# Kernel tuning notes

Measured on AMD Instinct MI355X. Metric: run time of the kernel, lower is better.

## Reference

```python
import jax, jax.numpy as jnp
import numpy as np

R = 4          # args.search_range
D = 2 * R + 1  # window size per axis -> D*D = 81 output channels


def setup_inputs() -> dict:
    key = jax.random.key(0)
    k1, k2 = jax.random.split(key)
    B, C, H, W = 4, 128, 64, 128
    src = jax.random.normal(k1, (B, C, H, W), dtype=jnp.float32)
    tgt = jax.random.normal(k2, (B, C, H, W), dtype=jnp.float32)
    return {"src": src, "tgt": tgt}


def reference(src, tgt):
    # Faithful to the torch code: tgt is zero-padded by R on each spatial side,
    # then for output pixel (i, j) the window indices into the PADDED tensor are
    # I in [i-R, i+R], J in [j-R, j+R]. For i < R the index is negative, which in
    # torch wraps around -> reproduce with modular indexing.
    B, C, H, W = src.shape
    tp = jnp.pad(tgt, ((0, 0), (0, 0), (R, R), (R, R)))  # [B,C,H+2R,W+2R]
    Hp, Wp = H + 2 * R, W + 2 * R
    # col_idx[dj, j] = (j - R + dj) mod Wp
    col_idx = (jnp.arange(W)[None, :] - R + jnp.arange(D)[:, None]) % Wp  # [D,W]
    outs = []
    for di in range(D):  # small fixed loop over 9 row offsets
        row_idx = (jnp.arange(H) - R + di) % Hp        # [H]
        t_rows = tp[:, :, row_idx, :]                  # [B,C,H,Wp]
        t_win = t_rows[:, :, :, col_idx]               # [B,C,H,D,W]
        # channel-dot-product per pixel and per column offset
        outs.append(jnp.einsum('bchdw,bchw->bdhw', t_win, src))
    # channel ordering k = di*D + dj matches the original double loop over (I, J)
    return jnp.concatenate(outs, axis=1)  # [B, D*D, H, W]
```

## Files before the change

kernel.cpp:

```cpp
#include <hip/hip_runtime.h>
#include <stdint.h>

#define NB 4
#define NC 128
#define NH 64
#define NW 128
#define HW (NH * NW)
#define ND 9
#define NOUT (ND * ND)
#define PROW 1040

typedef __attribute__((ext_vector_type(8))) short short8;
typedef __attribute__((ext_vector_type(4))) float f32x4;

__device__ __forceinline__ ushort f2bf(float f) {
  uint u = __float_as_uint(f);
  u += 0x7FFFu + ((u >> 16) & 1u);
  return (ushort)(u >> 16);
}

__global__ __launch_bounds__(512, 2) void costvol_kernel(const float* __restrict__ src,
                                                         const float* __restrict__ tgt,
                                                         float* __restrict__ out) {
  __shared__ ushort srcP[16 * PROW];
  __shared__ ushort tgtP[2][16 * PROW];
  __shared__ float  outlds[ND * NW];

  const int tid  = threadIdx.x;
  const int lane = tid & 63;
  const int wave = tid >> 6;
  const int col  = lane & 15;
  const int g    = lane >> 4;

  const int xcd = blockIdx.x & 7;
  const int b   = xcd >> 1;
  const int h   = ((xcd & 1) << 5) | (blockIdx.x >> 3);

  const int sc = (tid >> 5) << 3;
  const int sn = (tid & 31) << 2;

  const float* sbase = src + (size_t)(b * NC) * HW;
  const float* tbase = tgt + (size_t)(b * NC) * HW;

  {
    float4 v[8];
#pragma unroll
    for (int j = 0; j < 8; ++j)
      v[j] = *(const float4*)(sbase + (size_t)(sc + j) * HW + h * NW + sn);
#pragma unroll
    for (int i = 0; i < 4; ++i) {
      short8 e;
#pragma unroll
      for (int j = 0; j < 8; ++j) e[j] = (short)f2bf(((const float*)&v[j])[i]);
      *(short8*)&srcP[(tid >> 5) * PROW + (sn + i) * 8] = e;
    }
  }
  {
    const int y0 = (h - 8 < 0) ? 0 : (h - 8);
    float4 v[8];
#pragma unroll
    for (int j = 0; j < 8; ++j)
      v[j] = *(const float4*)(tbase + (size_t)(sc + j) * HW + y0 * NW + sn);
#pragma unroll
    for (int i = 0; i < 4; ++i) {
      short8 e;
#pragma unroll
      for (int j = 0; j < 8; ++j) e[j] = (short)f2bf(((const float*)&v[j])[i]);
      *(short8*)&tgtP[0][(tid >> 5) * PROW + (sn + i) * 8] = e;
    }
  }
  __syncthreads();

  const int m0 = wave << 4;
  short8 A[4];
#pragma unroll
  for (int kk = 0; kk < 4; ++kk)
    A[kk] = *(const short8*)&srcP[(4 * kk + g) * PROW + (m0 + col) * 8];

  for (int di = 0; di < ND; ++di) {
    const int p = di & 1;
    const int y = h + di - 8;

    float4 v[8];
    const bool havenext = (di < 8);
    if (havenext) {
      const int yn = (y + 1 < 0) ? 0 : (y + 1);
#pragma unroll
      for (int j = 0; j < 8; ++j)
        v[j] = *(const float4*)(tbase + (size_t)(sc + j) * HW + yn * NW + sn);
    }

    if (y >= 0) {
      const ushort* tp = tgtP[p];
      short8 BD[4], BS[4];
#pragma unroll
      for (int kk = 0; kk < 4; ++kk)
        BD[kk] = *(const short8*)&tp[(4 * kk + g) * PROW + (m0 + col) * 8];
      if (wave) {
#pragma unroll
        for (int kk = 0; kk < 4; ++kk)
          BS[kk] = *(const short8*)&tp[(4 * kk + g) * PROW + (m0 - 16 + col) * 8];
      }

      f32x4 accD = {0.f, 0.f, 0.f, 0.f};
      f32x4 accS = {0.f, 0.f, 0.f, 0.f};
#pragma unroll
      for (int kk = 0; kk < 4; ++kk)
        accD = __builtin_amdgcn_mfma_f32_16x16x32_bf16(A[kk], BD[kk], accD, 0, 0, 0);
      if (wave) {
#pragma unroll
        for (int kk = 0; kk < 4; ++kk)
          accS = __builtin_amdgcn_mfma_f32_16x16x32_bf16(A[kk], BS[kk], accS, 0, 0, 0);
      }

#pragma unroll
      for (int q = 0; q < 4; ++q) {
        const int row = 4 * g + q;
        const int w   = m0 + row;
        const int djd = col - row + 8;
        if (djd >= 0 && djd <= 8)
          outlds[djd * NW + ((w + 4 * djd) & 127)] = accD[q];
        if (wave) {
          const int djs = col - row - 8;
          if (djs >= 0 && djs <= 8)
            outlds[djs * NW + ((w + 4 * djs) & 127)] = accS[q];
        }
      }
    }

    if (havenext) {
#pragma unroll
      for (int i = 0; i < 4; ++i) {
        short8 e;
#pragma unroll
        for (int j = 0; j < 8; ++j) e[j] = (short)f2bf(((const float*)&v[j])[i]);
        *(short8*)&tgtP[p ^ 1][(tid >> 5) * PROW + (sn + i) * 8] = e;
      }
    }

    __syncthreads();

    if (tid < ND * 32) {
      const int dj = tid >> 5;
      const int w  = (tid & 31) << 2;
      f32x4 o = *(const f32x4*)&outlds[dj * NW + ((w + 4 * dj) & 127)];
      const bool vb = (y >= 0);
#pragma unroll
      for (int i = 0; i < 4; ++i)
        if (!vb || (w + i + dj < 8)) o[i] = 0.f;
      *(f32x4*)(out + ((size_t)((b * NOUT + di * ND + dj) * NH + h)) * NW + w) = o;
    }
    __syncthreads();
  }
}

extern "C" void kernel_launch(void* const* d_in, const int* in_sizes, int n_in,
                              void* d_out, int out_size, void* d_ws, size_t ws_size,
                              hipStream_t stream) {
  const float* src = (const float*)d_in[0];
  const float* tgt = (const float*)d_in[1];
  float* out = (float*)d_out;
  costvol_kernel<<<dim3(NB * NH), dim3(512), 0, stream>>>(src, tgt, out);
}
```

Before: 87.32 us.

## Split into bf16 pre-conversion pass and per-row-offset cost volume kernel

Adds a first kernel that converts src and tgt to bf16 once into a workspace, laid out channel-interleaved per row plane. The cost volume kernel then launches one block per (batch, row, di) instead of one per (batch, row), loading its bf16 planes straight from global memory with no per-iteration staging or barriers. This removes the 9x redundant fp32 tgt loads and conversions and the serial di loop with its double buffering, and gives nine times more blocks for parallelism. In exchange it adds a second launch and a round trip of the converted data through the workspace.

```diff
diff --git a/kernel.cpp b/kernel.cpp
--- a/kernel.cpp
+++ b/kernel.cpp
@@ -8,7 +8,8 @@
 #define HW (NH * NW)
 #define ND 9
 #define NOUT (ND * ND)
-#define PROW 1040
+#define PLANE 16384
+#define TGT_OFF ((size_t)NB * NH * PLANE)
 
 typedef __attribute__((ext_vector_type(8))) short short8;
 typedef __attribute__((ext_vector_type(4))) float f32x4;
@@ -19,13 +20,39 @@
   return (ushort)(u >> 16);
 }
 
-__global__ __launch_bounds__(512, 2) void costvol_kernel(const float* __restrict__ src,
+__global__ __launch_bounds__(512, 2) void convert_kernel(const float* __restrict__ src,
                                                          const float* __restrict__ tgt,
+                                                         ushort* __restrict__ ws) {
+  __shared__ ushort pl[PLANE];
+  const int t   = blockIdx.x >> 8;
+  const int b   = (blockIdx.x >> 6) & 3;
+  const int row = blockIdx.x & 63;
+  const float* in = (t ? tgt : src) + (size_t)(b * NC) * HW + row * NW;
+  ushort* outp = ws + (t ? TGT_OFF : 0) + (size_t)(b * NH + row) * PLANE;
+
+#pragma unroll
+  for (int i = 0; i < 8; ++i) {
+    const int cell = i * 512 + threadIdx.x;
+    const int c0 = (cell >> 7) << 2;
+    const int w  = cell & 127;
+    ushort4 e;
+    e.x = f2bf(in[(size_t)(c0 + 0) * HW + w]);
+    e.y = f2bf(in[(size_t)(c0 + 1) * HW + w]);
+    e.z = f2bf(in[(size_t)(c0 + 2) * HW + w]);
+    e.w = f2bf(in[(size_t)(c0 + 3) * HW + w]);
+    *(ushort4*)&pl[(c0 >> 3) * 1024 + w * 8 + (c0 & 7)] = e;
+  }
+  __syncthreads();
+#pragma unroll
+  for (int i = 0; i < 4; ++i) {
+    const int idx = i * 512 + threadIdx.x;
+    *(uint4*)(outp + idx * 8) = *(const uint4*)&pl[idx * 8];
+  }
+}
+
+__global__ __launch_bounds__(512, 2) void costvol_kernel(const ushort* __restrict__ ws,
                                                          float* __restrict__ out) {
-  __shared__ ushort srcP[16 * PROW];
-  __shared__ ushort tgtP[2][16 * PROW];
-  __shared__ float  outlds[ND * NW];
-
+  __shared__ float outlds[ND * NW];
   const int tid  = threadIdx.x;
   const int lane = tid & 63;
   const int wave = tid >> 6;
@@ -33,124 +60,73 @@
   const int g    = lane >> 4;
 
   const int xcd = blockIdx.x & 7;
+  const int k   = blockIdx.x >> 3;
   const int b   = xcd >> 1;
-  const int h   = ((xcd & 1) << 5) | (blockIdx.x >> 3);
+  const int h   = ((xcd & 1) << 5) | (k / ND);
+  const int di  = k % ND;
+  const int y   = h + di - 8;
 
-  const int sc = (tid >> 5) << 3;
-  const int sn = (tid & 31) << 2;
+  if (y < 0) {
+    if (tid < ND * 32) {
+      const int dj = tid >> 5;
+      const int w  = (tid & 31) << 2;
+      f32x4 o = {0.f, 0.f, 0.f, 0.f};
+      *(f32x4*)(out + ((size_t)((b * NOUT + di * ND + dj) * NH + h)) * NW + w) = o;
+    }
+    return;
+  }
 
-  const float* sbase = src + (size_t)(b * NC) * HW;
-  const float* tbase = tgt + (size_t)(b * NC) * HW;
+  const ushort* ap = ws + (size_t)(b * NH + h) * PLANE;
+  const ushort* tp = ws + TGT_OFF + (size_t)(b * NH + y) * PLANE;
+  const int m0 = wave << 4;
 
-  {
-    float4 v[8];
+  short8 A[4], BD[4], BS[4];
 #pragma unroll
-    for (int j = 0; j < 8; ++j)
-      v[j] = *(const float4*)(sbase + (size_t)(sc + j) * HW + h * NW + sn);
+  for (int kk = 0; kk < 4; ++kk) {
+    const int off = (4 * kk + g) * 1024 + (m0 + col) * 8;
+    A[kk]  = *(const short8*)&ap[off];
+    BD[kk] = *(const short8*)&tp[off];
+  }
+  if (wave) {
 #pragma unroll
-    for (int i = 0; i < 4; ++i) {
-      short8 e;
+    for (int kk = 0; kk < 4; ++kk)
+      BS[kk] = *(const short8*)&tp[(4 * kk + g) * 1024 + (m0 - 16 + col) * 8];
+  }
+
+  f32x4 accD = {0.f, 0.f, 0.f, 0.f};
+  f32x4 accS = {0.f, 0.f, 0.f, 0.f};
 #pragma unroll
-      for (int j = 0; j < 8; ++j) e[j] = (short)f2bf(((const float*)&v[j])[i]);
-      *(short8*)&srcP[(tid >> 5) * PROW + (sn + i) * 8] = e;
-    }
+  for (int kk = 0; kk < 4; ++kk)
+    accD = __builtin_amdgcn_mfma_f32_16x16x32_bf16(A[kk], BD[kk], accD, 0, 0, 0);
+  if (wave) {
+#pragma unroll
+    for (int kk = 0; kk < 4; ++kk)
+      accS = __builtin_amdgcn_mfma_f32_16x16x32_bf16(A[kk], BS[kk], accS, 0, 0, 0);
   }
-  {
-    const int y0 = (h - 8 < 0) ? 0 : (h - 8);
-    float4 v[8];
+
 #pragma unroll
-    for (int j = 0; j < 8; ++j)
-      v[j] = *(const float4*)(tbase + (size_t)(sc + j) * HW + y0 * NW + sn);
-#pragma unroll
-    for (int i = 0; i < 4; ++i) {
-      short8 e;
-#pragma unroll
-      for (int j = 0; j < 8; ++j) e[j] = (short)f2bf(((const float*)&v[j])[i]);
-      *(short8*)&tgtP[0][(tid >> 5) * PROW + (sn + i) * 8] = e;
+  for (int q = 0; q < 4; ++q) {
+    const int row = 4 * g + q;
+    const int w   = m0 + row;
+    const int djd = col - row + 8;
+    if (djd >= 0 && djd <= 8)
+      outlds[djd * NW + ((w + 4 * djd) & 127)] = accD[q];
+    if (wave) {
+      const int djs = col - row - 8;
+      if (djs >= 0 && djs <= 8)
+        outlds[djs * NW + ((w + 4 * djs) & 127)] = accS[q];
     }
   }
   __syncthreads();
 
-  const int m0 = wave << 4;
-  short8 A[4];
+  if (tid < ND * 32) {
+    const int dj = tid >> 5;
+    const int w  = (tid & 31) << 2;
+    f32x4 o = *(const f32x4*)&outlds[dj * NW + ((w + 4 * dj) & 127)];
 #pragma unroll
-  for (int kk = 0; kk < 4; ++kk)
-    A[kk] = *(const short8*)&srcP[(4 * kk + g) * PROW + (m0 + col) * 8];
-
-  for (int di = 0; di < ND; ++di) {
-    const int p = di & 1;
-    const int y = h + di - 8;
-
-    float4 v[8];
-    const bool havenext = (di < 8);
-    if (havenext) {
-      const int yn = (y + 1 < 0) ? 0 : (y + 1);
-#pragma unroll
-      for (int j = 0; j < 8; ++j)
-        v[j] = *(const float4*)(tbase + (size_t)(sc + j) * HW + yn * NW + sn);
-    }
-
-    if (y >= 0) {
-      const ushort* tp = tgtP[p];
-      short8 BD[4], BS[4];
-#pragma unroll
-      for (int kk = 0; kk < 4; ++kk)
-        BD[kk] = *(const short8*)&tp[(4 * kk + g) * PROW + (m0 + col) * 8];
-      if (wave) {
-#pragma unroll
-        for (int kk = 0; kk < 4; ++kk)
-          BS[kk] = *(const short8*)&tp[(4 * kk + g) * PROW + (m0 - 16 + col) * 8];
-      }
-
-      f32x4 accD = {0.f, 0.f, 0.f, 0.f};
-      f32x4 accS = {0.f, 0.f, 0.f, 0.f};
-#pragma unroll
-      for (int kk = 0; kk < 4; ++kk)
-        accD = __builtin_amdgcn_mfma_f32_16x16x32_bf16(A[kk], BD[kk], accD, 0, 0, 0);
-      if (wave) {
-#pragma unroll
-        for (int kk = 0; kk < 4; ++kk)
-          accS = __builtin_amdgcn_mfma_f32_16x16x32_bf16(A[kk], BS[kk], accS, 0, 0, 0);
-      }
-
-#pragma unroll
-      for (int q = 0; q < 4; ++q) {
-        const int row = 4 * g + q;
-        const int w   = m0 + row;
-        const int djd = col - row + 8;
-        if (djd >= 0 && djd <= 8)
-          outlds[djd * NW + ((w + 4 * djd) & 127)] = accD[q];
-        if (wave) {
-          const int djs = col - row - 8;
-          if (djs >= 0 && djs <= 8)
-            outlds[djs * NW + ((w + 4 * djs) & 127)] = accS[q];
-        }
-      }
-    }
-
-    if (havenext) {
-#pragma unroll
-      for (int i = 0; i < 4; ++i) {
-        short8 e;
-#pragma unroll
-        for (int j = 0; j < 8; ++j) e[j] = (short)f2bf(((const float*)&v[j])[i]);
-        *(short8*)&tgtP[p ^ 1][(tid >> 5) * PROW + (sn + i) * 8] = e;
-      }
-    }
-
-    __syncthreads();
-
-    if (tid < ND * 32) {
-      const int dj = tid >> 5;
-      const int w  = (tid & 31) << 2;
-      f32x4 o = *(const f32x4*)&outlds[dj * NW + ((w + 4 * dj) & 127)];
-      const bool vb = (y >= 0);
-#pragma unroll
-      for (int i = 0; i < 4; ++i)
-        if (!vb || (w + i + dj < 8)) o[i] = 0.f;
-      *(f32x4*)(out + ((size_t)((b * NOUT + di * ND + dj) * NH + h)) * NW + w) = o;
-    }
-    __syncthreads();
+    for (int i = 0; i < 4; ++i)
+      if (w + i + dj < 8) o[i] = 0.f;
+    *(f32x4*)(out + ((size_t)((b * NOUT + di * ND + dj) * NH + h)) * NW + w) = o;
   }
 }
 
@@ -160,5 +136,7 @@
   const float* src = (const float*)d_in[0];
   const float* tgt = (const float*)d_in[1];
   float* out = (float*)d_out;
-  costvol_kernel<<<dim3(NB * NH), dim3(512), 0, stream>>>(src, tgt, out);
+  ushort* ws = (ushort*)d_ws;
+  convert_kernel<<<dim3(2 * NB * NH), dim3(512), 0, stream>>>(src, tgt, ws);
+  costvol_kernel<<<dim3(NB * NH * ND), dim3(512), 0, stream>>>(ws, out);
 }
```

After: 89.29 us. 1.02x slower.
